# Kernel tuning notes

Hardware: AMD Instinct MI355X
Metric: run time of the kernel (lower is better)

The kernel has to match this reference:

```python
import jax, jax.numpy as jnp
import numpy as np

NEG_INF = -1.0e9
LN_EPS = 1e-5
LEAK = 0.2


def setup_inputs() -> dict:
    key = jax.random.key(0)
    ks = jax.random.split(key, 8)
    B, C, T, N, H = 8, 64, 24, 512, 2
    hd = C // H
    x = jax.random.normal(ks[0], (B, C, T, N), dtype=jnp.float32)
    gso = jax.random.randint(ks[1], (N, N), 0, 2, dtype=jnp.int32)
    # torch nn.Linear weights are (out, in); xavier-ish scale
    s = (2.0 / (C + C)) ** 0.5
    Wq = jax.random.normal(ks[2], (C, C), dtype=jnp.float32) * s
    Wk = jax.random.normal(ks[3], (C, C), dtype=jnp.float32) * s
    Wv = jax.random.normal(ks[4], (C, C), dtype=jnp.float32) * s
    sa = (2.0 / (H + hd)) ** 0.5
    a_src = jax.random.normal(ks[5], (H, hd), dtype=jnp.float32) * sa
    a_dst = jax.random.normal(ks[6], (H, hd), dtype=jnp.float32) * sa
    ln_gamma = jnp.ones((C,), dtype=jnp.float32)
    ln_beta = jnp.zeros((C,), dtype=jnp.float32)
    return {"x": x, "gso": gso, "Wq": Wq, "Wk": Wk, "Wv": Wv,
            "a_src": a_src, "a_dst": a_dst, "ln_gamma": ln_gamma, "ln_beta": ln_beta}


def _spatial_gat(x, gso, Wq, Wk, Wv, a_src, a_dst, ln_gamma, ln_beta):
    B, C, T, N = x.shape
    H, hd = a_src.shape
    # (B, C, T, N) -> (B*T, N, C)
    xr = jnp.transpose(x, (0, 2, 3, 1)).reshape(B * T, N, C)
    # torch Linear: y = x @ W.T
    Q = jnp.einsum('bnc,dc->bnd', xr, Wq).reshape(B * T, N, H, hd)
    K = jnp.einsum('bnc,dc->bnd', xr, Wk).reshape(B * T, N, H, hd)
    V = jnp.einsum('bnc,dc->bnd', xr, Wv).reshape(B * T, N, H, hd)
    # additive GAT scores, all heads at once
    s_src = jnp.einsum('bnhd,hd->bnh', Q, a_src)  # (BT, N, H)
    s_dst = jnp.einsum('bnhd,hd->bnh', K, a_dst)  # (BT, N, H)
    scores = jax.nn.leaky_relu(s_src[:, :, None, :] + s_dst[:, None, :, :], LEAK)  # (BT, Ni, Nj, H)
    mask = jnp.where(gso == 0, jnp.float32(NEG_INF), jnp.float32(0.0))  # (N, N)
    scores = scores + mask[None, :, :, None]
    attn = jax.nn.softmax(scores, axis=2)  # softmax over destination j
    out = jnp.einsum('bijh,bjhd->bihd', attn, V)  # (BT, N, H, hd)
    out = out.reshape(B * T, N, C)
    # LayerNorm over channel dim
    mu = jnp.mean(out, axis=-1, keepdims=True)
    var = jnp.var(out, axis=-1, keepdims=True)
    out = (out - mu) * jax.lax.rsqrt(var + LN_EPS) * ln_gamma + ln_beta
    # back to (B, C, T, N)
    return jnp.transpose(out.reshape(B, T, N, C), (0, 3, 1, 2))


def reference(x, gso, Wq, Wk, Wv, a_src, a_dst, ln_gamma, ln_beta):
    return _spatial_gat(x, gso, Wq, Wk, Wv, a_src, a_dst, ln_gamma, ln_beta)
```

## Files before the change

### kernel.cpp

```cpp
#include <hip/hip_runtime.h>

#define CDIM 64
#define TDIM 24
#define NDIM 512
#define NBT  192

typedef float    float4v __attribute__((ext_vector_type(4)));
typedef _Float16 half8v  __attribute__((ext_vector_type(8)));
typedef _Float16 half4v  __attribute__((ext_vector_type(4)));
typedef _Float16 half2v  __attribute__((ext_vector_type(2)));


__device__ __forceinline__ float exp2_fast(float x) {
#if __has_builtin(__builtin_amdgcn_exp2f)
  return __builtin_amdgcn_exp2f(x);
#else
  return __expf(x * 0.69314718f);
#endif
}

struct SmemK1 {
  union {
    _Float16 xt[128][72];
    _Float16 vtb[64][136];
  } big;
  _Float16 wv[64][72];
  _Float16 wext[16][72];
};

__launch_bounds__(256, 4)
__global__ void k1_v(const float* __restrict__ x,  const float* __restrict__ Wv,
                     const float* __restrict__ Wq, const float* __restrict__ Wk,
                     const float* __restrict__ a_src, const float* __restrict__ a_dst,
                     const int* __restrict__ gso,
                     _Float16* __restrict__ VT_g,
                     _Float16* __restrict__ F16, _Float16* __restrict__ P16,
                     _Float16* __restrict__ E16, _Float16* __restrict__ Q16,
                     unsigned char* __restrict__ maskb) {
  const int t  = threadIdx.x;
  const int bx = blockIdx.x;

  if (bx >= 768) {
    int g = (bx - 768) * 256 + t;
    const int4* gp = (const int4*)gso + (size_t)g * 4;
    unsigned w[4];
#pragma unroll
    for (int k = 0; k < 4; ++k) {
      int4 v = gp[k];
      w[k] = (v.x ? 0x000000FFu : 0u) | (v.y ? 0x0000FF00u : 0u) |
             (v.z ? 0x00FF0000u : 0u) | (v.w ? 0xFF000000u : 0u);
    }
    uint4 o; o.x = w[0]; o.y = w[1]; o.z = w[2]; o.w = w[3];
    ((uint4*)maskb)[g] = o;
    return;
  }

  __shared__ SmemK1 sm;
  const int qn = bx & 3;
  const int bt = bx >> 2;
  const int b  = bt / TDIM, tt = bt % TDIM;
  const int n0 = qn * 128;

#pragma unroll
  for (int it = 0; it < 4; ++it) {
    int idx = it * 256 + t;
    float4 vv = ((const float4*)Wv)[idx];
    int d = idx >> 4, k4 = (idx & 15) * 4;
    half4v h4; h4[0] = (_Float16)vv.x; h4[1] = (_Float16)vv.y;
    h4[2] = (_Float16)vv.z; h4[3] = (_Float16)vv.w;
    *(half4v*)&sm.wv[d][k4] = h4;
  }
  for (int z = t; z < 12 * 72; z += 256) ((_Float16*)sm.wext[4])[z] = (_Float16)0.f;
  if (t < 64) {
    int c = t;
    float s0 = 0.f, s1 = 0.f, d0 = 0.f, d1 = 0.f;
#pragma unroll
    for (int d = 0; d < 32; ++d) {
      s0 += a_src[d]      * Wq[d * 64 + c];
      s1 += a_src[32 + d] * Wq[(32 + d) * 64 + c];
      d0 += a_dst[d]      * Wk[d * 64 + c];
      d1 += a_dst[32 + d] * Wk[(32 + d) * 64 + c];
    }
    const float l2e = 1.44269504f;
    sm.wext[0][c] = (_Float16)(s0 * l2e); sm.wext[1][c] = (_Float16)(s1 * l2e);
    sm.wext[2][c] = (_Float16)(d0 * l2e); sm.wext[3][c] = (_Float16)(d1 * l2e);
  }
  for (int it = 0; it < 16; ++it) {
    int idx = it * 256 + t;
    int cp = idx >> 7, n = idx & 127;
    int c0 = cp * 2;
    const float* base = x + ((size_t)(b * CDIM + c0) * TDIM + tt) * NDIM + n0 + n;
    half2v p; p[0] = (_Float16)base[0]; p[1] = (_Float16)base[(size_t)TDIM * NDIM];
    *(half2v*)&sm.big.xt[n][c0] = p;
  }
  __syncthreads();

  const int lane = t & 63, w = t >> 6;
  const int m = lane & 15, quad = lane >> 4;
  const int mbase = w * 32;

  float4v acc[2][5];
#pragma unroll
  for (int mt = 0; mt < 2; ++mt)
#pragma unroll
    for (int nt = 0; nt < 5; ++nt)
#pragma unroll
      for (int r = 0; r < 4; ++r) acc[mt][nt][r] = 0.f;

#pragma unroll
  for (int ks = 0; ks < 2; ++ks) {
    half8v af[2], bf[5];
#pragma unroll
    for (int mt = 0; mt < 2; ++mt)
      af[mt] = *(const half8v*)&sm.big.xt[mbase + mt * 16 + m][ks * 32 + quad * 8];
#pragma unroll
    for (int nt = 0; nt < 4; ++nt)
      bf[nt] = *(const half8v*)&sm.wv[nt * 16 + m][ks * 32 + quad * 8];
    bf[4] = *(const half8v*)&sm.wext[m][ks * 32 + quad * 8];
#pragma unroll
    for (int mt = 0; mt < 2; ++mt)
#pragma unroll
      for (int nt = 0; nt < 5; ++nt)
        acc[mt][nt] = __builtin_amdgcn_mfma_f32_16x16x32_f16(af[mt], bf[nt], acc[mt][nt], 0, 0, 0);
  }

  if (m < 4) {
    const int hh = m & 1;
    const bool is_src = (m < 2);
    _Float16* eb = (is_src ? E16 : F16) + ((size_t)(bt * 2 + hh)) * NDIM;
    _Float16* qb = (is_src ? Q16 : P16) + ((size_t)(bt * 2 + hh)) * NDIM;
    const float bias = is_src ? -6.f : 0.f;
#pragma unroll
    for (int mt = 0; mt < 2; ++mt)
#pragma unroll
      for (int r = 0; r < 4; ++r) {
        float s = acc[mt][4][r];
        int n = n0 + mbase + mt * 16 + quad * 4 + r;
        eb[n] = (_Float16)exp2_fast(s + bias);
        qb[n] = (_Float16)exp2_fast(0.2f * s + bias);
      }
  }
  __syncthreads();

#pragma unroll
  for (int mt = 0; mt < 2; ++mt)
#pragma unroll
    for (int nt = 0; nt < 4; ++nt)
#pragma unroll
      for (int r = 0; r < 4; r += 2) {
        int nl = mbase + mt * 16 + quad * 4 + r;
        int c  = nt * 16 + m;
        half2v p = __builtin_bit_cast(half2v,
            __builtin_amdgcn_cvt_pkrtz(acc[mt][nt][r], acc[mt][nt][r + 1]));
        *(half2v*)&sm.big.vtb[c][nl] = p;
      }
  __syncthreads();

  const uint4* vq = (const uint4*)sm.big.vtb;
#pragma unroll
  for (int it = 0; it < 4; ++it) {
    int idx = it * 256 + t;
    int c = idx >> 4, q4 = idx & 15;
    ((uint4*)VT_g)[(size_t)(bt * 64 + c) * 64 + qn * 16 + q4] = vq[c * 17 + q4];
  }
}

struct SmemK2 {
  union {
    struct { _Float16 vt[64][128]; } s;
    struct { float otile[128][66]; float rsum[2][128]; float rsq[2][128];
             float mu[128]; float rs[128]; } e;
  } u;
  _Float16 sF16[2][512];
  _Float16 sP16[2][512];
};

__launch_bounds__(256, 4)
__global__ void k2_attn(const _Float16* __restrict__ VT_g,
                        const _Float16* __restrict__ F16, const _Float16* __restrict__ P16,
                        const _Float16* __restrict__ E16, const _Float16* __restrict__ Q16,
                        const unsigned char* __restrict__ maskb,
                        const float* __restrict__ gamma, const float* __restrict__ beta,
                        float* __restrict__ out) {
  __shared__ SmemK2 sm;
  const int t     = threadIdx.x;
  const int id    = blockIdx.x;
  const int itile = (id >> 3) & 3;
  const int bt    = ((id >> 5) << 3) | (id & 7);
  const int i0    = itile * 128;
  const int b     = bt / TDIM, tt = bt % TDIM;
  const int lane  = t & 63, w = t >> 6;
  const int h = w >> 1, ihalf = w & 1;
  const int m = lane & 15, quad = lane >> 4;
  const int rbase = ihalf * 64;

  {
    uint2 fv = ((const uint2*)(F16 + (size_t)bt * 2 * NDIM))[t];
    uint2 pw = ((const uint2*)(P16 + (size_t)bt * 2 * NDIM))[t];
    ((uint2*)sm.sF16)[t] = fv;
    ((uint2*)sm.sP16)[t] = pw;
  }
  half2v e2[4], q2[4];
  {
    const _Float16* eb = E16 + ((size_t)(bt * 2 + h)) * NDIM + i0 + rbase + m;
    const _Float16* qb = Q16 + ((size_t)(bt * 2 + h)) * NDIM + i0 + rbase + m;
#pragma unroll
    for (int mt = 0; mt < 4; ++mt) {
      _Float16 ev = eb[mt * 16];
      _Float16 qv = qb[mt * 16];
      e2[mt][0] = ev; e2[mt][1] = ev;
      q2[mt][0] = qv; q2[mt][1] = qv;
    }
  }

  float4v acc[4][2], accs[4];
#pragma unroll
  for (int mt = 0; mt < 4; ++mt)
#pragma unroll
    for (int r = 0; r < 4; ++r) { acc[mt][0][r] = 0.f; acc[mt][1][r] = 0.f; accs[mt][r] = 0.f; }
  const half8v bones = {(_Float16)1.f, (_Float16)1.f, (_Float16)1.f, (_Float16)1.f,
                        (_Float16)1.f, (_Float16)1.f, (_Float16)1.f, (_Float16)1.f};

  const uint4* vsrc = (const uint4*)VT_g;
  uint4 pv0, pv1, pv2, pv3;
  const int vc  = t >> 4;
  const int vch = t & 15;
  const int vswz = (vch * 8) ^ ((vc & 7) * 8);

  const unsigned char* mrow = maskb + (size_t)(i0 + rbase + m) * NDIM + quad * 8;

#define PREFETCH_A(js_)                                                        \
  { pv0 = vsrc[(size_t)(bt * 64 + vc     ) * 64 + (js_) * 16 + vch];           \
    pv1 = vsrc[(size_t)(bt * 64 + vc + 16) * 64 + (js_) * 16 + vch]; }
#define PREFETCH_B(js_)                                                        \
  { pv2 = vsrc[(size_t)(bt * 64 + vc + 32) * 64 + (js_) * 16 + vch];           \
    pv3 = vsrc[(size_t)(bt * 64 + vc + 48) * 64 + (js_) * 16 + vch]; }

#define SLICE(js_, ksl_)                                                       \
  {                                                                            \
    const int jq = (ksl_) * 32 + quad * 8;                                     \
    half8v F8 = *(const half8v*)&sm.sF16[h][(js_) * 128 + jq];                 \
    half8v P8 = *(const half8v*)&sm.sP16[h][(js_) * 128 + jq];                 \
    const int vbase = (h * 32 + m) * 128 + (jq ^ ((m & 7) * 8));               \
    half8v b0 = *(const half8v*)&sm.u.s.vt[0][vbase];                          \
    half8v b1 = *(const half8v*)&sm.u.s.vt[0][vbase + 16 * 128];               \
    uint4 fu = __builtin_bit_cast(uint4, F8);                                  \
    uint4 pu = __builtin_bit_cast(uint4, P8);                                  \
    half2v f2a = __builtin_bit_cast(half2v, fu.x), f2b = __builtin_bit_cast(half2v, fu.y); \
    half2v f2c = __builtin_bit_cast(half2v, fu.z), f2d = __builtin_bit_cast(half2v, fu.w); \
    half2v p2a = __builtin_bit_cast(half2v, pu.x), p2b = __builtin_bit_cast(half2v, pu.y); \
    half2v p2c = __builtin_bit_cast(half2v, pu.z), p2d = __builtin_bit_cast(half2v, pu.w); \
    _Pragma("unroll")                                                          \
    for (int mt = 0; mt < 4; ++mt) {                                           \
      unsigned mw0 = mk[mt][ksl_].x, mw1 = mk[mt][ksl_].y;                     \
      uint4 eu;                                                                \
      eu.x = __builtin_bit_cast(unsigned,                                      \
               __builtin_elementwise_max(e2[mt] * f2a, q2[mt] * p2a)) &        \
             __builtin_amdgcn_perm(0u, mw0, 0x01010000u);                      \
      eu.y = __builtin_bit_cast(unsigned,                                      \
               __builtin_elementwise_max(e2[mt] * f2b, q2[mt] * p2b)) &        \
             __builtin_amdgcn_perm(0u, mw0, 0x03030202u);                      \
      eu.z = __builtin_bit_cast(unsigned,                                      \
               __builtin_elementwise_max(e2[mt] * f2c, q2[mt] * p2c)) &        \
             __builtin_amdgcn_perm(0u, mw1, 0x01010000u);                      \
      eu.w = __builtin_bit_cast(unsigned,                                      \
               __builtin_elementwise_max(e2[mt] * f2d, q2[mt] * p2d)) &        \
             __builtin_amdgcn_perm(0u, mw1, 0x03030202u);                      \
      half8v af = __builtin_bit_cast(half8v, eu);                              \
      acc[mt][0] = __builtin_amdgcn_mfma_f32_16x16x32_f16(af, b0,    acc[mt][0], 0, 0, 0); \
      acc[mt][1] = __builtin_amdgcn_mfma_f32_16x16x32_f16(af, b1,    acc[mt][1], 0, 0, 0); \
      accs[mt]   = __builtin_amdgcn_mfma_f32_16x16x32_f16(af, bones, accs[mt],   0, 0, 0); \
    }                                                                          \
  }

  PREFETCH_A(0);
  PREFETCH_B(0);

#pragma unroll
  for (int js = 0; js < 4; ++js) {
    __syncthreads();
    *(uint4*)&sm.u.s.vt[vc     ][vswz] = pv0;
    *(uint4*)&sm.u.s.vt[vc + 16][vswz] = pv1;
    *(uint4*)&sm.u.s.vt[vc + 32][vswz] = pv2;
    *(uint4*)&sm.u.s.vt[vc + 48][vswz] = pv3;
    __syncthreads();
    if (js < 3) PREFETCH_A(js + 1);

    uint2 mk[4][4];
#pragma unroll
    for (int mt = 0; mt < 4; ++mt) {
      const unsigned char* mbp = mrow + (size_t)(mt * 16) * NDIM + js * 128;
#pragma unroll
      for (int ksl = 0; ksl < 4; ++ksl)
        mk[mt][ksl] = *(const uint2*)(mbp + ksl * 32);
    }

    SLICE(js, 0);
    SLICE(js, 1);
    if (js < 3) PREFETCH_B(js + 1);
    SLICE(js, 2);
    SLICE(js, 3);
  }
#undef SLICE
#undef PREFETCH_A
#undef PREFETCH_B

  __syncthreads();
#pragma unroll
  for (int mt = 0; mt < 4; ++mt)
#pragma unroll
    for (int r = 0; r < 4; ++r) {
      float sc = __builtin_amdgcn_rcpf(accs[mt][r]);
      int i_loc = rbase + mt * 16 + quad * 4 + r;
#pragma unroll
      for (int nt = 0; nt < 2; ++nt)
        sm.u.e.otile[i_loc][h * 32 + nt * 16 + m] = acc[mt][nt][r] * sc;
    }
  __syncthreads();

  {
    int i = t & 127, cg = t >> 7;
    float s1 = 0.f, s2 = 0.f;
#pragma unroll
    for (int cc = 0; cc < 32; ++cc) {
      float v = sm.u.e.otile[i][cg * 32 + cc];
      s1 += v; s2 += v * v;
    }
    sm.u.e.rsum[cg][i] = s1;
    sm.u.e.rsq[cg][i]  = s2;
  }
  __syncthreads();
  if (t < 128) {
    int i = t;
    float s1 = sm.u.e.rsum[0][i] + sm.u.e.rsum[1][i];
    float s2 = sm.u.e.rsq[0][i]  + sm.u.e.rsq[1][i];
    float mu  = s1 * (1.f / 64.f);
    float var = s2 * (1.f / 64.f) - mu * mu;
    sm.u.e.mu[i] = mu;
    sm.u.e.rs[i] = rsqrtf(var + 1e-5f);
  }
  __syncthreads();
  {
    int i = t & 127, cg = t >> 7;
    float mu = sm.u.e.mu[i], rs = sm.u.e.rs[i];
    int n = i0 + i;
#pragma unroll
    for (int cc = 0; cc < 32; ++cc) {
      int c = cg * 32 + cc;
      float v = (sm.u.e.otile[i][c] - mu) * rs * gamma[c] + beta[c];
      out[((size_t)(b * CDIM + c) * TDIM + tt) * NDIM + n] = v;
    }
  }
}

extern "C" void kernel_launch(void* const* d_in, const int* in_sizes, int n_in,
                              void* d_out, int out_size, void* d_ws, size_t ws_size,
                              hipStream_t stream) {
  const float* x     = (const float*)d_in[0];
  const int*   gso   = (const int*)d_in[1];
  const float* Wq    = (const float*)d_in[2];
  const float* Wk    = (const float*)d_in[3];
  const float* Wv    = (const float*)d_in[4];
  const float* a_src = (const float*)d_in[5];
  const float* a_dst = (const float*)d_in[6];
  const float* gamma = (const float*)d_in[7];
  const float* beta  = (const float*)d_in[8];
  float* out = (float*)d_out;

  char* ws = (char*)d_ws;
  _Float16* VT_g = (_Float16*)ws;
  _Float16* F16  = (_Float16*)(ws + 12582912);
  _Float16* P16  = (_Float16*)(ws + 12976128);
  _Float16* E16  = (_Float16*)(ws + 13369344);
  _Float16* Q16  = (_Float16*)(ws + 13762560);
  unsigned char* maskb = (unsigned char*)(ws + 14155776);

  k1_v<<<832, 256, 0, stream>>>(x, Wv, Wq, Wk, a_src, a_dst, gso,
                                VT_g, F16, P16, E16, Q16, maskb);
  k2_attn<<<768, 256, 0, stream>>>(VT_g, F16, P16, E16, Q16, maskb,
                                   gamma, beta, out);
}
```

Baseline: 122.8 us.

## Double-buffer V tile in LDS and drop one barrier per j-step

Doubles the shared-memory V tile so the next j-slice can be written into the alternate buffer while the current one is consumed, cutting the two barriers per iteration down to one. All four V prefetches are issued at the top of each iteration, and mask bytes for the next slice are loaded after the compute. Launch bounds drop from 4 to 3 blocks per SM. The larger LDS footprint and lower occupancy target may cut latency hiding from concurrent blocks, and the mask loads now sit on the critical path before the barrier.

```diff
diff --git a/kernel.cpp b/kernel.cpp
--- a/kernel.cpp
+++ b/kernel.cpp
@@ -167,7 +167,7 @@
 
 struct SmemK2 {
   union {
-    struct { _Float16 vt[64][128]; } s;
+    struct { _Float16 vt[2][64][128]; } s;
     struct { float otile[128][66]; float rsum[2][128]; float rsq[2][128];
              float mu[128]; float rs[128]; } e;
   } u;
@@ -175,7 +175,7 @@
   _Float16 sP16[2][512];
 };
 
-__launch_bounds__(256, 4)
+__launch_bounds__(256, 3)
 __global__ void k2_attn(const _Float16* __restrict__ VT_g,
                         const _Float16* __restrict__ F16, const _Float16* __restrict__ P16,
                         const _Float16* __restrict__ E16, const _Float16* __restrict__ Q16,
@@ -228,22 +228,37 @@
   const int vswz = (vch * 8) ^ ((vc & 7) * 8);
 
   const unsigned char* mrow = maskb + (size_t)(i0 + rbase + m) * NDIM + quad * 8;
-
-#define PREFETCH_A(js_)                                                        \
+  uint2 mk[4][4];
+
+#define PREFETCH_V(js_)                                                        \
   { pv0 = vsrc[(size_t)(bt * 64 + vc     ) * 64 + (js_) * 16 + vch];           \
-    pv1 = vsrc[(size_t)(bt * 64 + vc + 16) * 64 + (js_) * 16 + vch]; }
-#define PREFETCH_B(js_)                                                        \
-  { pv2 = vsrc[(size_t)(bt * 64 + vc + 32) * 64 + (js_) * 16 + vch];           \
+    pv1 = vsrc[(size_t)(bt * 64 + vc + 16) * 64 + (js_) * 16 + vch];           \
+    pv2 = vsrc[(size_t)(bt * 64 + vc + 32) * 64 + (js_) * 16 + vch];           \
     pv3 = vsrc[(size_t)(bt * 64 + vc + 48) * 64 + (js_) * 16 + vch]; }
 
-#define SLICE(js_, ksl_)                                                       \
+#define PREFETCH_M(js_)                                                        \
+  { _Pragma("unroll")                                                          \
+    for (int mt = 0; mt < 4; ++mt) {                                           \
+      const unsigned char* mbp = mrow + (size_t)(mt * 16) * NDIM + (js_) * 128;\
+      _Pragma("unroll")                                                        \
+      for (int ksl = 0; ksl < 4; ++ksl)                                        \
+        mk[mt][ksl] = *(const uint2*)(mbp + ksl * 32);                         \
+    } }
+
+#define COMMIT(buf_)                                                           \
+  { *(uint4*)&sm.u.s.vt[buf_][vc     ][vswz] = pv0;                            \
+    *(uint4*)&sm.u.s.vt[buf_][vc + 16][vswz] = pv1;                            \
+    *(uint4*)&sm.u.s.vt[buf_][vc + 32][vswz] = pv2;                            \
+    *(uint4*)&sm.u.s.vt[buf_][vc + 48][vswz] = pv3; }
+
+#define SLICE(buf_, js_, ksl_)                                                 \
   {                                                                            \
     const int jq = (ksl_) * 32 + quad * 8;                                     \
     half8v F8 = *(const half8v*)&sm.sF16[h][(js_) * 128 + jq];                 \
     half8v P8 = *(const half8v*)&sm.sP16[h][(js_) * 128 + jq];                 \
     const int vbase = (h * 32 + m) * 128 + (jq ^ ((m & 7) * 8));               \
-    half8v b0 = *(const half8v*)&sm.u.s.vt[0][vbase];                          \
-    half8v b1 = *(const half8v*)&sm.u.s.vt[0][vbase + 16 * 128];               \
+    half8v b0 = *(const half8v*)&sm.u.s.vt[buf_][0][vbase];                    \
+    half8v b1 = *(const half8v*)&sm.u.s.vt[buf_][0][vbase + 16 * 128];         \
     uint4 fu = __builtin_bit_cast(uint4, F8);                                  \
     uint4 pu = __builtin_bit_cast(uint4, P8);                                  \
     half2v f2a = __builtin_bit_cast(half2v, fu.x), f2b = __builtin_bit_cast(half2v, fu.y); \
@@ -273,37 +288,29 @@
     }                                                                          \
   }
 
-  PREFETCH_A(0);
-  PREFETCH_B(0);
+  PREFETCH_V(0);
+  PREFETCH_M(0);
+  COMMIT(0);
+  __syncthreads();
 
 #pragma unroll
   for (int js = 0; js < 4; ++js) {
-    __syncthreads();
-    *(uint4*)&sm.u.s.vt[vc     ][vswz] = pv0;
-    *(uint4*)&sm.u.s.vt[vc + 16][vswz] = pv1;
-    *(uint4*)&sm.u.s.vt[vc + 32][vswz] = pv2;
-    *(uint4*)&sm.u.s.vt[vc + 48][vswz] = pv3;
-    __syncthreads();
-    if (js < 3) PREFETCH_A(js + 1);
-
-    uint2 mk[4][4];
-#pragma unroll
-    for (int mt = 0; mt < 4; ++mt) {
-      const unsigned char* mbp = mrow + (size_t)(mt * 16) * NDIM + js * 128;
-#pragma unroll
-      for (int ksl = 0; ksl < 4; ++ksl)
-        mk[mt][ksl] = *(const uint2*)(mbp + ksl * 32);
-    }
-
-    SLICE(js, 0);
-    SLICE(js, 1);
-    if (js < 3) PREFETCH_B(js + 1);
-    SLICE(js, 2);
-    SLICE(js, 3);
+    const int cur = js & 1, nxt = cur ^ 1;
+    if (js < 3) PREFETCH_V(js + 1);
+    SLICE(cur, js, 0);
+    SLICE(cur, js, 1);
+    SLICE(cur, js, 2);
+    SLICE(cur, js, 3);
+    if (js < 3) {
+      PREFETCH_M(js + 1);
+      COMMIT(nxt);
+      __syncthreads();
+    }
   }
 #undef SLICE
-#undef PREFETCH_A
-#undef PREFETCH_B
+#undef COMMIT
+#undef PREFETCH_M
+#undef PREFETCH_V
 
   __syncthreads();
 #pragma unroll
```

After: 124.4 us. Within noise of the previous version (+1.4%).

## Read V fragments directly from global memory instead of staging through LDS

Applied to the files above, without the earlier changes.

The attention kernel no longer stages V tiles through shared memory with double-buffered register prefetch and per-chunk barriers. Each lane now loads its MFMA B operands straight from global/L2, and the F/P vectors move into the shared-memory union so LDS use shrinks. Launch bounds drop from 4 to 3 blocks per SM, giving more registers per thread. This removes the LDS write/read traffic and the barriers inside the loop, but it relies on cache hits and loses the explicit prefetch overlap.

```diff
diff --git a/kernel.cpp b/kernel.cpp
--- a/kernel.cpp
+++ b/kernel.cpp
@@ -167,15 +167,13 @@
 
 struct SmemK2 {
   union {
-    struct { _Float16 vt[64][128]; } s;
+    struct { _Float16 sF16[2][512]; _Float16 sP16[2][512]; } f;
     struct { float otile[128][66]; float rsum[2][128]; float rsq[2][128];
              float mu[128]; float rs[128]; } e;
   } u;
-  _Float16 sF16[2][512];
-  _Float16 sP16[2][512];
 };
 
-__launch_bounds__(256, 4)
+__launch_bounds__(256, 3)
 __global__ void k2_attn(const _Float16* __restrict__ VT_g,
                         const _Float16* __restrict__ F16, const _Float16* __restrict__ P16,
                         const _Float16* __restrict__ E16, const _Float16* __restrict__ Q16,
@@ -197,8 +195,8 @@
   {
     uint2 fv = ((const uint2*)(F16 + (size_t)bt * 2 * NDIM))[t];
     uint2 pw = ((const uint2*)(P16 + (size_t)bt * 2 * NDIM))[t];
-    ((uint2*)sm.sF16)[t] = fv;
-    ((uint2*)sm.sP16)[t] = pw;
+    ((uint2*)sm.u.f.sF16)[t] = fv;
+    ((uint2*)sm.u.f.sP16)[t] = pw;
   }
   half2v e2[4], q2[4];
   {
@@ -221,29 +219,22 @@
   const half8v bones = {(_Float16)1.f, (_Float16)1.f, (_Float16)1.f, (_Float16)1.f,
                         (_Float16)1.f, (_Float16)1.f, (_Float16)1.f, (_Float16)1.f};
 
-  const uint4* vsrc = (const uint4*)VT_g;
-  uint4 pv0, pv1, pv2, pv3;
-  const int vc  = t >> 4;
-  const int vch = t & 15;
-  const int vswz = (vch * 8) ^ ((vc & 7) * 8);
-
-  const unsigned char* mrow = maskb + (size_t)(i0 + rbase + m) * NDIM + quad * 8;
-
-#define PREFETCH_A(js_)                                                        \
-  { pv0 = vsrc[(size_t)(bt * 64 + vc     ) * 64 + (js_) * 16 + vch];           \
-    pv1 = vsrc[(size_t)(bt * 64 + vc + 16) * 64 + (js_) * 16 + vch]; }
-#define PREFETCH_B(js_)                                                        \
-  { pv2 = vsrc[(size_t)(bt * 64 + vc + 32) * 64 + (js_) * 16 + vch];           \
-    pv3 = vsrc[(size_t)(bt * 64 + vc + 48) * 64 + (js_) * 16 + vch]; }
+  const _Float16* vr0 = VT_g + ((size_t)(bt * 64 + h * 32 + m)) * NDIM + quad * 8;
+  const _Float16* vr1 = vr0 + (size_t)16 * NDIM;
+  const unsigned char* mr0 = maskb + (size_t)(i0 + rbase + m) * NDIM + quad * 8;
+  const unsigned char* mr1 = mr0 + (size_t)16 * NDIM;
+  const unsigned char* mr2 = mr0 + (size_t)32 * NDIM;
+  const unsigned char* mr3 = mr0 + (size_t)48 * NDIM;
+
+  __syncthreads();
 
 #define SLICE(js_, ksl_)                                                       \
   {                                                                            \
     const int jq = (ksl_) * 32 + quad * 8;                                     \
-    half8v F8 = *(const half8v*)&sm.sF16[h][(js_) * 128 + jq];                 \
-    half8v P8 = *(const half8v*)&sm.sP16[h][(js_) * 128 + jq];                 \
-    const int vbase = (h * 32 + m) * 128 + (jq ^ ((m & 7) * 8));               \
-    half8v b0 = *(const half8v*)&sm.u.s.vt[0][vbase];                          \
-    half8v b1 = *(const half8v*)&sm.u.s.vt[0][vbase + 16 * 128];               \
+    half8v F8 = *(const half8v*)&sm.u.f.sF16[h][(js_) * 128 + jq];             \
+    half8v P8 = *(const half8v*)&sm.u.f.sP16[h][(js_) * 128 + jq];             \
+    half8v b0 = *(const half8v*)(vr0 + (js_) * 128 + (ksl_) * 32);             \
+    half8v b1 = *(const half8v*)(vr1 + (js_) * 128 + (ksl_) * 32);             \
     uint4 fu = __builtin_bit_cast(uint4, F8);                                  \
     uint4 pu = __builtin_bit_cast(uint4, P8);                                  \
     half2v f2a = __builtin_bit_cast(half2v, fu.x), f2b = __builtin_bit_cast(half2v, fu.y); \
@@ -273,37 +264,22 @@
     }                                                                          \
   }
 
-  PREFETCH_A(0);
-  PREFETCH_B(0);
-
 #pragma unroll
   for (int js = 0; js < 4; ++js) {
-    __syncthreads();
-    *(uint4*)&sm.u.s.vt[vc     ][vswz] = pv0;
-    *(uint4*)&sm.u.s.vt[vc + 16][vswz] = pv1;
-    *(uint4*)&sm.u.s.vt[vc + 32][vswz] = pv2;
-    *(uint4*)&sm.u.s.vt[vc + 48][vswz] = pv3;
-    __syncthreads();
-    if (js < 3) PREFETCH_A(js + 1);
-
     uint2 mk[4][4];
 #pragma unroll
-    for (int mt = 0; mt < 4; ++mt) {
-      const unsigned char* mbp = mrow + (size_t)(mt * 16) * NDIM + js * 128;
-#pragma unroll
-      for (int ksl = 0; ksl < 4; ++ksl)
-        mk[mt][ksl] = *(const uint2*)(mbp + ksl * 32);
-    }
-
+    for (int ksl = 0; ksl < 4; ++ksl) {
+      mk[0][ksl] = *(const uint2*)(mr0 + js * 128 + ksl * 32);
+      mk[1][ksl] = *(const uint2*)(mr1 + js * 128 + ksl * 32);
+      mk[2][ksl] = *(const uint2*)(mr2 + js * 128 + ksl * 32);
+      mk[3][ksl] = *(const uint2*)(mr3 + js * 128 + ksl * 32);
+    }
     SLICE(js, 0);
     SLICE(js, 1);
-    if (js < 3) PREFETCH_B(js + 1);
     SLICE(js, 2);
     SLICE(js, 3);
   }
 #undef SLICE
-#undef PREFETCH_A
-#undef PREFETCH_B
 
   __syncthreads();
 #pragma unroll
```

Result: slower. 131.4 us (+7.0%).
